# Optimization experiments

Hardware: AMD Instinct MI355X
Metric: run time of the kernel (lower is better)

Reference implementation:

```python
import jax, jax.numpy as jnp
import numpy as np

B, N, F_IN, OUT, H, D = 8, 1024, 256, 256, 2, 4  # D = 4 directions U,D,R,L


def setup_inputs() -> dict:
    key = jax.random.key(0)
    kx, kW, ka, *kA = jax.random.split(key, 7)
    x = jax.random.normal(kx, (B, N, F_IN), dtype=jnp.float32)
    # Stacked per-direction, per-head Linear weights (no bias): (D, H, in, out)
    W = jax.random.normal(kW, (D, H, F_IN, OUT), dtype=jnp.float32) / np.sqrt(F_IN)
    # Stacked attention vectors: (D, H, 2*out)
    a = jax.random.normal(ka, (D, H, 2 * OUT), dtype=jnp.float32) / np.sqrt(OUT)
    ks = jax.random.split(kA[0], 4)
    A_U, A_D, A_R, A_L = [jax.random.randint(k, (N, N), 0, 2, dtype=jnp.int32) for k in ks]
    # guarantee every row has at least one neighbor so softmax rows are finite
    A_U = A_U.at[jnp.arange(N), jnp.arange(N)].set(1)
    return {"x": x, "A_U": A_U, "A_D": A_D, "A_R": A_R, "A_L": A_L, "W": W, "a": a}


def reference(x, A_U, A_D, A_R, A_L, W, a):
    num_heads = W.shape[1]
    out_dim = W.shape[3]
    A = jnp.stack([A_U, A_D, A_R, A_L])  # (D, N, N), order U,D,R,L as in forward
    # All direction/head projections in one einsum: (D,H,B,N,out)
    Wh = jnp.einsum('bnf,dhfo->dhbno', x, W)
    e_src = jnp.einsum('dhbno,dho->dhbn', Wh, a[:, :, :out_dim])
    e_dst = jnp.einsum('dhbno,dho->dhbn', Wh, a[:, :, out_dim:])
    # e[d,h,b,i,j] = leaky_relu(e_src[d,h,b,i] + e_dst[d,h,b,j])
    e = jax.nn.leaky_relu(e_src[..., :, None] + e_dst[..., None, :], negative_slope=0.01)
    # Sequential where-merge: later (d,h) overwrite earlier where A[d] != 0,
    # exactly matching torch's loop order (within a direction only last head survives).
    e_total = jnp.full(e.shape[2:], -jnp.inf, dtype=x.dtype)  # (B,N,N)
    for d in range(4):
        mask = (A[d] != 0)[None]  # (1,N,N)
        for h in range(num_heads):
            e_total = jnp.where(mask, e[d, h], e_total)
    alpha = jax.nn.softmax(e_total, axis=2)  # (B,N,N)
    # out = sum_d sum_h (alpha*A_d) @ Wh[d,h]  =  sum_d (alpha*A_d) @ sum_h Wh[d,h]
    Wh_sum = Wh.sum(axis=1)  # (D,B,N,out)
    Af = A.astype(x.dtype)
    out = jnp.einsum('dij,bij,dbjo->bio', Af, alpha, Wh_sum) / num_heads
    return out
```

## Files before the change

kernel.cpp:

```cpp
#include <hip/hip_runtime.h>

#define B_ 8
#define N_ 1024
#define F_ 256
#define O_ 256

typedef unsigned short u16;
typedef unsigned int u32;
typedef __attribute__((ext_vector_type(8))) short bf8;
typedef __attribute__((ext_vector_type(4))) float f4;

__device__ __forceinline__ u16 f2bf(float f) {
  union { float f; u32 u; } c; c.f = f;
  u32 u = c.u;
  u32 r = u + 0x7FFFu + ((u >> 16) & 1u);
  return (u16)(r >> 16);
}
__device__ __forceinline__ float bf2f(u16 u) {
  union { u32 i; float f; } c; c.i = ((u32)u) << 16; return c.f;
}

#if defined(__has_builtin)
#if __has_builtin(__builtin_amdgcn_perm)
#define HAVE_PERM 1
#endif
#endif
__device__ __forceinline__ u32 dup01(u32 e) {
#ifdef HAVE_PERM
  return __builtin_amdgcn_perm(e, e, 0x01010000u);
#else
  return (e & 0xFFu) * 0x0101u + (e & 0xFF00u) * 0x010100u;
#endif
}
__device__ __forceinline__ u32 dup23(u32 e) {
#ifdef HAVE_PERM
  return __builtin_amdgcn_perm(e, e, 0x03030202u);
#else
  return ((e >> 16) & 0xFFu) * 0x0101u + ((e >> 16) & 0xFF00u) * 0x010100u;
#endif
}

__global__ __launch_bounds__(256) void k_prep(const float* __restrict__ W,
                                              const float* __restrict__ a,
                                              u16* __restrict__ Wt,
                                              float* __restrict__ vsrc,
                                              float* __restrict__ vdst,
                                              const int* __restrict__ AU,
                                              const int* __restrict__ AD,
                                              const int* __restrict__ AR,
                                              const int* __restrict__ AL,
                                              unsigned char* __restrict__ nibR,
                                              unsigned char* __restrict__ nibF) {
  __shared__ u16 t[64][72];
  __shared__ float red[2][4];
  int bx = blockIdx.x;
  int tdx = threadIdx.x;
  if (bx < 64) {
    int d = bx >> 4, tile = bx & 15;
    int f0 = (tile >> 2) * 64, o0 = (tile & 3) * 64;
    const float* src0 = W + (d * 2 + 0) * 65536;
    const float* src1 = W + (d * 2 + 1) * 65536;
    u16* dst = Wt + d * 65536;
    for (int i = 0; i < 2; ++i) {
      int c = i * 256 + tdx;
      int row = c >> 3, cc = (c & 7) * 8;
      int base = (f0 + row) * 256 + o0 + cc;
      float4 a0 = *(const float4*)&src0[base];
      float4 a1 = *(const float4*)&src0[base + 4];
      float4 b0 = *(const float4*)&src1[base];
      float4 b1 = *(const float4*)&src1[base + 4];
      u16 tmp[8] __attribute__((aligned(16)));
      tmp[0] = f2bf(a0.x + b0.x); tmp[1] = f2bf(a0.y + b0.y);
      tmp[2] = f2bf(a0.z + b0.z); tmp[3] = f2bf(a0.w + b0.w);
      tmp[4] = f2bf(a1.x + b1.x); tmp[5] = f2bf(a1.y + b1.y);
      tmp[6] = f2bf(a1.z + b1.z); tmp[7] = f2bf(a1.w + b1.w);
      *(uint4*)&t[row][cc] = *(uint4*)tmp;
    }
    __syncthreads();
    for (int i = 0; i < 2; ++i) {
      int c = i * 256 + tdx;
      int orow = c >> 3, fc = (c & 7) * 8;
      u16 v[8] __attribute__((aligned(16)));
#pragma unroll
      for (int k = 0; k < 8; ++k) v[k] = t[fc + k][orow];
      *(uint4*)&dst[(o0 + orow) * 256 + f0 + fc] = *(uint4*)v;
    }
  } else if (bx < 1088) {
    int blk = bx - 64;
    int d = blk >> 8, f = blk & 255;
    int o = tdx;
    int dh = d * 2 + 1;
    float w = W[(dh * 256 + f) * 256 + o];
    float as = a[dh * 512 + o];
    float ad = a[dh * 512 + 256 + o];
    float ps = w * as, pd = w * ad;
    for (int off = 32; off; off >>= 1) {
      ps += __shfl_down(ps, off);
      pd += __shfl_down(pd, off);
    }
    int lane = o & 63, w4 = o >> 6;
    if (lane == 0) { red[0][w4] = ps; red[1][w4] = pd; }
    __syncthreads();
    if (o == 0) vsrc[d * 256 + f] = red[0][0] + red[0][1] + red[0][2] + red[0][3];
    if (o == 1) vdst[d * 256 + f] = red[1][0] + red[1][1] + red[1][2] + red[1][3];
  } else {
    int idx = (bx - 1088) * 256 + tdx;
    int i = idx >> 7;
    int jb = (idx & 127) * 8;
    int base = i * 1024 + jb;
    int4 au0 = *(const int4*)&AU[base], au1 = *(const int4*)&AU[base + 4];
    int4 ad0 = *(const int4*)&AD[base], ad1 = *(const int4*)&AD[base + 4];
    int4 ar0 = *(const int4*)&AR[base], ar1 = *(const int4*)&AR[base + 4];
    int4 al0 = *(const int4*)&AL[base], al1 = *(const int4*)&AL[base + 4];
    int u[8] = {au0.x, au0.y, au0.z, au0.w, au1.x, au1.y, au1.z, au1.w};
    int dn[8] = {ad0.x, ad0.y, ad0.z, ad0.w, ad1.x, ad1.y, ad1.z, ad1.w};
    int rr[8] = {ar0.x, ar0.y, ar0.z, ar0.w, ar1.x, ar1.y, ar1.z, ar1.w};
    int ll[8] = {al0.x, al0.y, al0.z, al0.w, al1.x, al1.y, al1.z, al1.w};
    unsigned char m[8] __attribute__((aligned(8)));
#pragma unroll
    for (int k = 0; k < 8; ++k)
      m[k] = (unsigned char)((u[k] ? 1u : 0u) | (dn[k] ? 2u : 0u) | (rr[k] ? 4u : 0u) | (ll[k] ? 8u : 0u));
    *(uint2*)&nibR[base] = *(uint2*)m;
    int it = i >> 4, jw = jb >> 5;
    int lane = ((jb >> 3) & 3) * 16 + (i & 15);
    *(uint2*)&nibF[((it * 32 + jw) * 64 + lane) * 8] = *(uint2*)m;
  }
}

__global__ __launch_bounds__(256) void k_edots(const float* __restrict__ x,
                                               const float* __restrict__ vsrc,
                                               const float* __restrict__ vdst,
                                               float* __restrict__ es,
                                               float* __restrict__ ed,
                                               u16* __restrict__ xb) {
  int t = threadIdx.x, lane = t & 63, w = t >> 6;
  int f4i = lane * 4;
  float4 vs[4], vd[4];
#pragma unroll
  for (int d = 0; d < 4; ++d) {
    vs[d] = *(const float4*)&vsrc[d * 256 + f4i];
    vd[d] = *(const float4*)&vdst[d * 256 + f4i];
  }
  int row0 = blockIdx.x * 16 + w * 4;
  for (int rr = 0; rr < 4; ++rr) {
    int row = row0 + rr;
    float4 xv = *(const float4*)&x[(size_t)row * 256 + f4i];
    u16 pk[4] __attribute__((aligned(8)));
    pk[0] = f2bf(xv.x); pk[1] = f2bf(xv.y); pk[2] = f2bf(xv.z); pk[3] = f2bf(xv.w);
    *(uint2*)&xb[(size_t)row * 256 + f4i] = *(uint2*)pk;
    float p[8];
#pragma unroll
    for (int d = 0; d < 4; ++d) {
      p[d] = xv.x * vs[d].x + xv.y * vs[d].y + xv.z * vs[d].z + xv.w * vs[d].w;
      p[4 + d] = xv.x * vd[d].x + xv.y * vd[d].y + xv.z * vd[d].z + xv.w * vd[d].w;
    }
#pragma unroll
    for (int v = 0; v < 8; ++v)
      for (int off = 32; off; off >>= 1) p[v] += __shfl_xor(p[v], off);
    if (lane == 0) {
      int b = row >> 10, n = row & 1023;
#pragma unroll
      for (int d = 0; d < 4; ++d) {
        es[(d * 8 + b) * 1024 + n] = p[d];
        ed[(d * 8 + b) * 1024 + n] = p[4 + d];
      }
    }
  }
}

__global__ __launch_bounds__(256, 2) void k_mid(const u16* __restrict__ X,
                                                const u16* __restrict__ Wt,
                                                u16* __restrict__ WhstF,
                                                const float* __restrict__ es,
                                                const float* __restrict__ ed,
                                                const unsigned char* __restrict__ nibR,
                                                u16* __restrict__ alphaF) {
  __shared__ char smem[51200];
  int bx = blockIdx.x;
  int t = threadIdx.x;
  int lane = t & 63, w = t >> 6;
  if (bx < 512) {
    u16* lA = (u16*)smem;
    u16* lB = (u16*)(smem + 8192);
    u16* sC = (u16*)(smem + 16384);
    int xo = bx & 1;
    int m0 = ((bx >> 1) & 63) * 128;
    int d = bx >> 7;
    int o0 = xo * 128;
    int wm = w >> 1, wn = w & 1;
    int r16 = lane & 15, quad = lane >> 4, q8 = quad * 8;
    f4 acc[4][4];
    const f4 fz = {0.f, 0.f, 0.f, 0.f};
#pragma unroll
    for (int i = 0; i < 4; ++i)
#pragma unroll
      for (int j = 0; j < 4; ++j) acc[i][j] = fz;

    const u16* Bp = Wt + d * 65536;
    for (int k0 = 0; k0 < 256; k0 += 32) {
      uint4 va[2], vb[2];
#pragma unroll
      for (int i = 0; i < 2; ++i) {
        int c = i * 256 + t;
        int row = c >> 2, ko = (c & 3) * 8;
        va[i] = *(const uint4*)&X[(size_t)(m0 + row) * 256 + k0 + ko];
        vb[i] = *(const uint4*)&Bp[(o0 + row) * 256 + k0 + ko];
      }
      __syncthreads();
#pragma unroll
      for (int i = 0; i < 2; ++i) {
        int c = i * 256 + t;
        *(uint4*)&lA[c * 8] = va[i];
        *(uint4*)&lB[c * 8] = vb[i];
      }
      __syncthreads();
      bf8 af[4], bfr[4];
#pragma unroll
      for (int tm = 0; tm < 4; ++tm)
        af[tm] = *(const bf8*)&lA[(wm * 64 + tm * 16 + r16) * 32 + q8];
#pragma unroll
      for (int tn = 0; tn < 4; ++tn)
        bfr[tn] = *(const bf8*)&lB[(wn * 64 + tn * 16 + r16) * 32 + q8];
#pragma unroll
      for (int tm = 0; tm < 4; ++tm)
#pragma unroll
        for (int tn = 0; tn < 4; ++tn)
          acc[tm][tn] = __builtin_amdgcn_mfma_f32_16x16x32_bf16(
              af[tm], bfr[tn], acc[tm][tn], 0, 0, 0);
    }
#pragma unroll
    for (int tm = 0; tm < 4; ++tm) {
#pragma unroll
      for (int tn = 0; tn < 4; ++tn) {
        int o = wn * 64 + tn * 16 + r16;
        int n = wm * 64 + tm * 16 + quad * 4;
        u16 p[4] __attribute__((aligned(8)));
#pragma unroll
        for (int r = 0; r < 4; ++r) p[r] = f2bf(acc[tm][tn][r]);
        *(uint2*)&sC[o * 136 + n] = *(uint2*)p;
      }
    }
    __syncthreads();
    int b = m0 >> 10;
    int nlo = m0 & 1023;
    int dbbase = d * 8 + b;
    int otg0 = o0 >> 4, jwg0 = nlo >> 5;
#pragma unroll
    for (int cc = 0; cc < 8; ++cc) {
      int c = cc * 256 + t;
      int p = c >> 6, l = c & 63;
      int ot_l = p >> 2, jw_l = p & 3;
      int o_l = ot_l * 16 + (l & 15);
      int j_l = jw_l * 32 + (l >> 4) * 8;
      uint4 v = *(const uint4*)&sC[o_l * 136 + j_l];
      int off = (((dbbase * 16 + otg0 + ot_l) * 32 + jwg0 + jw_l) * 64 + l) * 8;
      *(uint4*)&WhstF[off] = v;
    }
  } else {
    float* sEd = (float*)smem;
    u16 (*sAl)[1032] = (u16(*)[1032])(smem + 16384);
    float* srs = (float*)(smem + 49408);
    int sx = bx - 512;
    int it = sx & 63, b = sx >> 6;
    const float NINF = -__builtin_inff();
#pragma unroll
    for (int c = 0; c < 4; ++c) {
      int q = c * 256 + t;
      int d = q >> 8, jc = (q & 255) * 4;
      *(float4*)&sEd[d * 1024 + jc] = *(const float4*)&ed[(size_t)(d * 8 + b) * 1024 + jc];
    }
    __syncthreads();
    for (int rr = 0; rr < 4; ++rr) {
      int r = w * 4 + rr;
      int i = it * 16 + r;
      float e0 = es[(0 * 8 + b) * 1024 + i];
      float e1 = es[(1 * 8 + b) * 1024 + i];
      float e2 = es[(2 * 8 + b) * 1024 + i];
      float e3 = es[(3 * 8 + b) * 1024 + i];
      unsigned mbv[16];
#pragma unroll
      for (int k = 0; k < 16; ++k) mbv[k] = nibR[i * 1024 + k * 64 + lane];
      float e[16];
      float mx = NINF;
#pragma unroll
      for (int k = 0; k < 16; ++k) {
        unsigned m = mbv[k];
        int d = m ? (31 - __clz((int)m)) : 0;
        float esd = d == 0 ? e0 : d == 1 ? e1 : d == 2 ? e2 : e3;
        float z = esd + sEd[d * 1024 + k * 64 + lane];
        float lz = z > 0.0f ? z : 0.01f * z;
        e[k] = m ? lz : NINF;
        mx = fmaxf(mx, e[k]);
      }
      for (int off = 32; off; off >>= 1) mx = fmaxf(mx, __shfl_xor(mx, off));
      float s = 0.f;
#pragma unroll
      for (int k = 0; k < 16; ++k) {
        float p = exp2f((e[k] - mx) * 1.4426950408889634f);
        s += p;
        sAl[r][k * 64 + lane] = f2bf(p);
      }
      for (int off = 32; off; off >>= 1) s += __shfl_xor(s, off);
      if (lane == 0) srs[r] = 1.0f / s;
    }
    __syncthreads();
#pragma unroll
    for (int cc = 0; cc < 8; ++cc) {
      int c = cc * 256 + t;
      int jw = c >> 6, l = c & 63;
      int i_l = l & 15;
      int j_l = jw * 32 + (l >> 4) * 8;
      uint4 v = *(const uint4*)&sAl[i_l][j_l];
      float rs = srs[i_l];
      u16 pk[8] __attribute__((aligned(16)));
      u32 wv[4] = {v.x, v.y, v.z, v.w};
#pragma unroll
      for (int k = 0; k < 4; ++k) {
        pk[k * 2] = f2bf(bf2f((u16)(wv[k] & 0xFFFFu)) * rs);
        pk[k * 2 + 1] = f2bf(bf2f((u16)(wv[k] >> 16)) * rs);
      }
      int off = (((b * 64 + it) * 32 + jw) * 64 + l) * 8;
      *(uint4*)&alphaF[off] = *(uint4*)pk;
    }
  }
}

__global__ __launch_bounds__(256, 2) void k_agg(const u16* __restrict__ alphaF,
                                                const unsigned char* __restrict__ nibF,
                                                const u16* __restrict__ WhstF,
                                                u16* __restrict__ part) {
  int ob2 = blockIdx.x;
  int bz = blockIdx.y;
  int iz = blockIdx.z;
  int b = bz >> 2, ks = bz & 3;
  int t = threadIdx.x, lane = t & 63, w = t >> 6;
  int wm = w >> 1, wn = w & 1;
  int r16 = lane & 15, quad = lane >> 4;
  int itb = iz * 8 + wm * 4;
  int otb = ob2 * 8 + wn * 4;
  int jw0 = ks * 8;

  int aoff[4], noff[4], bo[4];
#pragma unroll
  for (int tm = 0; tm < 4; ++tm) {
    aoff[tm] = (((b * 64 + itb + tm) * 32 + jw0) * 64 + lane) * 8;
    noff[tm] = (((itb + tm) * 32 + jw0) * 64 + lane) * 8;
  }
#pragma unroll
  for (int d = 0; d < 4; ++d)
    bo[d] = ((((d * 8 + b) * 16 + otb) * 32 + jw0) * 64 + lane) * 8;

  f4 acc[4][4];
  const f4 fz = {0.f, 0.f, 0.f, 0.f};
#pragma unroll
  for (int i = 0; i < 4; ++i)
#pragma unroll
    for (int j = 0; j < 4; ++j) acc[i][j] = fz;

  uint4 A[2][4];
  uint2 Nn[2][4];
  uint4 Bb[4][4];
  union U { uint4 u; bf8 h; };

#pragma unroll
  for (int tm = 0; tm < 4; ++tm) {
    A[0][tm] = *(const uint4*)&alphaF[aoff[tm]];
    Nn[0][tm] = *(const uint2*)&nibF[noff[tm]];
  }
#pragma unroll
  for (int s = 0; s < 3; ++s)
#pragma unroll
    for (int tn = 0; tn < 4; ++tn)
      Bb[s][tn] = *(const uint4*)&WhstF[bo[s & 3] + (s >> 2) * 512 + tn * 16384];

#pragma unroll
  for (int js = 0; js < 8; ++js) {
    int cs = js & 1;
    if (js < 7) {
#pragma unroll
      for (int tm = 0; tm < 4; ++tm) {
        A[cs ^ 1][tm] = *(const uint4*)&alphaF[aoff[tm] + (js + 1) * 512];
        Nn[cs ^ 1][tm] = *(const uint2*)&nibF[noff[tm] + (js + 1) * 512];
      }
    }
#pragma unroll
    for (int d = 0; d < 4; ++d) {
      int s = js * 4 + d;
      if (s + 3 < 32) {
        int js3 = (s + 3) >> 2, d3 = (s + 3) & 3;
#pragma unroll
        for (int tn = 0; tn < 4; ++tn)
          Bb[(s + 3) & 3][tn] = *(const uint4*)&WhstF[bo[d3] + js3 * 512 + tn * 16384];
      }
      U af[4];
#pragma unroll
      for (int tm = 0; tm < 4; ++tm) {
        uint2 mb = Nn[cs][tm];
        u32 e0 = ((mb.x >> d) & 0x01010101u) * 0xFFu;
        u32 e1 = ((mb.y >> d) & 0x01010101u) * 0xFFu;
        af[tm].u.x = A[cs][tm].x & dup01(e0);
        af[tm].u.y = A[cs][tm].y & dup23(e0);
        af[tm].u.z = A[cs][tm].z & dup01(e1);
        af[tm].u.w = A[cs][tm].w & dup23(e1);
      }
#pragma unroll
      for (int tm = 0; tm < 4; ++tm)
#pragma unroll
        for (int tn = 0; tn < 4; ++tn) {
          U bb; bb.u = Bb[s & 3][tn];
          acc[tm][tn] = __builtin_amdgcn_mfma_f32_16x16x32_bf16(
              af[tm].h, bb.h, acc[tm][tn], 0, 0, 0);
        }
    }
  }
  u16* P = part + (size_t)ks * 2097152;
#pragma unroll
  for (int tm = 0; tm < 4; ++tm) {
#pragma unroll
    for (int tn = 0; tn < 4; ++tn) {
      int irow = (itb + tm) * 16 + quad * 4;
      int go = (otb + tn) * 16 + r16;
#pragma unroll
      for (int r = 0; r < 4; ++r)
        P[((size_t)b * 1024 + irow + r) * 256 + go] = f2bf(acc[tm][tn][r]);
    }
  }
}

__global__ void k_reduce(const u16* __restrict__ part, float* __restrict__ out) {
  int idx = (blockIdx.x * 256 + threadIdx.x) * 8;
  float s[8];
#pragma unroll
  for (int k = 0; k < 8; ++k) s[k] = 0.f;
#pragma unroll
  for (int ks = 0; ks < 4; ++ks) {
    uint4 v = *(const uint4*)&part[(size_t)ks * 2097152 + idx];
    u32 ww[4] = {v.x, v.y, v.z, v.w};
#pragma unroll
    for (int k = 0; k < 4; ++k) {
      union { u32 i; float f; } lo, hi;
      lo.i = (ww[k] & 0xFFFFu) << 16;
      hi.i = ww[k] & 0xFFFF0000u;
      s[k * 2] += lo.f;
      s[k * 2 + 1] += hi.f;
    }
  }
  float4 o0 = {0.5f * s[0], 0.5f * s[1], 0.5f * s[2], 0.5f * s[3]};
  float4 o1 = {0.5f * s[4], 0.5f * s[5], 0.5f * s[6], 0.5f * s[7]};
  *(float4*)&out[idx] = o0;
  *(float4*)&out[idx + 4] = o1;
}

extern "C" void kernel_launch(void* const* d_in, const int* in_sizes, int n_in,
                              void* d_out, int out_size, void* d_ws, size_t ws_size,
                              hipStream_t stream) {
  const float* x = (const float*)d_in[0];
  const int* AU = (const int*)d_in[1];
  const int* AD = (const int*)d_in[2];
  const int* AR = (const int*)d_in[3];
  const int* AL = (const int*)d_in[4];
  const float* W = (const float*)d_in[5];
  const float* a = (const float*)d_in[6];
  float* out = (float*)d_out;

  char* ws = (char*)d_ws;
  u16* Wt = (u16*)(ws + 0);
  float* vsrc = (float*)(ws + 524288);
  float* vdst = (float*)(ws + 528384);
  float* es = (float*)(ws + 532480);
  float* ed = (float*)(ws + 663552);
  unsigned char* nibR = (unsigned char*)(ws + 794624);
  unsigned char* nibF = (unsigned char*)(ws + 1843200);
  u16* xb = (u16*)(ws + 2891776);
  u16* WhstF = (u16*)(ws + 7086080);
  u16* alphaF = (u16*)(ws + 23863296);
  u16* part = (u16*)(ws + 40640512);
  if (ws_size < 57417728) return;

  hipLaunchKernelGGL(k_prep, dim3(1600), dim3(256), 0, stream,
                     W, a, Wt, vsrc, vdst, AU, AD, AR, AL, nibR, nibF);
  hipLaunchKernelGGL(k_edots, dim3(512), dim3(256), 0, stream, x, vsrc, vdst, es, ed, xb);
  hipLaunchKernelGGL(k_mid, dim3(1024), dim3(256), 0, stream,
                     xb, Wt, WhstF, es, ed, nibR, alphaF);
  hipLaunchKernelGGL(k_agg, dim3(2, 32, 8), dim3(256), 0, stream, alphaF, nibF, WhstF, part);
  hipLaunchKernelGGL(k_reduce, dim3(1024), dim3(256), 0, stream, part, out);
}
```

Baseline: 150.5 us.

## Stage Wh tiles in double-buffered LDS shared across waves in k_agg

Each wave loads the Wh B-operand for one direction and all eight output tiles into a double-buffered LDS array, with a register prefetch two steps ahead. All waves then read their B fragments from LDS, replacing per-wave redundant global loads. Before this, the two wm waves each fetched the same B tiles from global memory. The change removes that duplication and cuts global traffic, but adds LDS stores and reads plus a block-wide barrier on every j step, which may reduce overlap.

```diff
diff --git a/kernel.cpp b/kernel.cpp
--- a/kernel.cpp
+++ b/kernel.cpp
@@ -329,6 +329,7 @@
                                                 const unsigned char* __restrict__ nibF,
                                                 const u16* __restrict__ WhstF,
                                                 u16* __restrict__ part) {
+  __shared__ u16 ldsB[2][4][8][512];
   int ob2 = blockIdx.x;
   int bz = blockIdx.y;
   int iz = blockIdx.z;
@@ -337,18 +338,18 @@
   int wm = w >> 1, wn = w & 1;
   int r16 = lane & 15, quad = lane >> 4;
   int itb = iz * 8 + wm * 4;
-  int otb = ob2 * 8 + wn * 4;
   int jw0 = ks * 8;
 
-  int aoff[4], noff[4], bo[4];
+  int aoff[4], noff[4];
 #pragma unroll
   for (int tm = 0; tm < 4; ++tm) {
     aoff[tm] = (((b * 64 + itb + tm) * 32 + jw0) * 64 + lane) * 8;
     noff[tm] = (((itb + tm) * 32 + jw0) * 64 + lane) * 8;
   }
-#pragma unroll
-  for (int d = 0; d < 4; ++d)
-    bo[d] = ((((d * 8 + b) * 16 + otb) * 32 + jw0) * 64 + lane) * 8;
+  size_t gb[8];
+#pragma unroll
+  for (int ot = 0; ot < 8; ++ot)
+    gb[ot] = ((((size_t)(w * 8 + b) * 16 + ob2 * 8 + ot) * 32 + jw0) * 64 + lane) * 8;
 
   f4 acc[4][4];
   const f4 fz = {0.f, 0.f, 0.f, 0.f};
@@ -359,19 +360,21 @@
 
   uint4 A[2][4];
   uint2 Nn[2][4];
-  uint4 Bb[4][4];
+  uint4 vb[8];
   union U { uint4 u; bf8 h; };
 
+#pragma unroll
+  for (int ot = 0; ot < 8; ++ot) vb[ot] = *(const uint4*)&WhstF[gb[ot]];
+#pragma unroll
+  for (int ot = 0; ot < 8; ++ot) *(uint4*)&ldsB[0][w][ot][lane * 8] = vb[ot];
+#pragma unroll
+  for (int ot = 0; ot < 8; ++ot) vb[ot] = *(const uint4*)&WhstF[gb[ot] + 512];
 #pragma unroll
   for (int tm = 0; tm < 4; ++tm) {
     A[0][tm] = *(const uint4*)&alphaF[aoff[tm]];
     Nn[0][tm] = *(const uint2*)&nibF[noff[tm]];
   }
-#pragma unroll
-  for (int s = 0; s < 3; ++s)
-#pragma unroll
-    for (int tn = 0; tn < 4; ++tn)
-      Bb[s][tn] = *(const uint4*)&WhstF[bo[s & 3] + (s >> 2) * 512 + tn * 16384];
+  __syncthreads();
 
 #pragma unroll
   for (int js = 0; js < 8; ++js) {
@@ -385,14 +388,10 @@
     }
 #pragma unroll
     for (int d = 0; d < 4; ++d) {
-      int s = js * 4 + d;
-      if (s + 3 < 32) {
-        int js3 = (s + 3) >> 2, d3 = (s + 3) & 3;
-#pragma unroll
-        for (int tn = 0; tn < 4; ++tn)
-          Bb[(s + 3) & 3][tn] = *(const uint4*)&WhstF[bo[d3] + js3 * 512 + tn * 16384];
-      }
-      U af[4];
+      U af[4], bfr[4];
+#pragma unroll
+      for (int tn = 0; tn < 4; ++tn)
+        bfr[tn].h = *(const bf8*)&ldsB[cs][d][wn * 4 + tn][lane * 8];
 #pragma unroll
       for (int tm = 0; tm < 4; ++tm) {
         uint2 mb = Nn[cs][tm];
@@ -406,14 +405,23 @@
 #pragma unroll
       for (int tm = 0; tm < 4; ++tm)
 #pragma unroll
-        for (int tn = 0; tn < 4; ++tn) {
-          U bb; bb.u = Bb[s & 3][tn];
+        for (int tn = 0; tn < 4; ++tn)
           acc[tm][tn] = __builtin_amdgcn_mfma_f32_16x16x32_bf16(
-              af[tm].h, bb.h, acc[tm][tn], 0, 0, 0);
-        }
-    }
+              af[tm].h, bfr[tn].h, acc[tm][tn], 0, 0, 0);
+    }
+    if (js < 7) {
+#pragma unroll
+      for (int ot = 0; ot < 8; ++ot) *(uint4*)&ldsB[cs ^ 1][w][ot][lane * 8] = vb[ot];
+      if (js + 2 < 8) {
+#pragma unroll
+        for (int ot = 0; ot < 8; ++ot)
+          vb[ot] = *(const uint4*)&WhstF[gb[ot] + (size_t)(js + 2) * 512];
+      }
+    }
+    __syncthreads();
   }
   u16* P = part + (size_t)ks * 2097152;
+  int otb = ob2 * 8 + wn * 4;
 #pragma unroll
   for (int tm = 0; tm < 4; ++tm) {
 #pragma unroll
```

Result: slower. 174.0 us (+15.7%).
